# Performance work log

Hardware: AMD Instinct MI355X
Metric: run time of the kernel (lower is better)

Reference implementation:

```python
import jax, jax.numpy as jnp
import numpy as np

D_MODEL = 1024
N_HEADS = 16
D_HEAD = D_MODEL // N_HEADS


def setup_inputs() -> dict:
    key = jax.random.key(0)
    kx, kq, kk, kv = jax.random.split(key, 4)
    B, T = 2, 2048
    X = jax.random.normal(kx, (B, T, D_MODEL), dtype=jnp.float32)
    s = 1.0 / np.sqrt(D_MODEL)
    # torch nn.Linear weight is [out, in]; y = x @ W.T
    Wq = jax.random.uniform(kq, (D_MODEL, D_MODEL), jnp.float32, -s, s)
    Wk = jax.random.uniform(kk, (D_MODEL, D_MODEL), jnp.float32, -s, s)
    Wv = jax.random.uniform(kv, (D_MODEL, D_MODEL), jnp.float32, -s, s)
    return {"X": X, "Wq": Wq, "Wk": Wk, "Wv": Wv}


def reference(X, Wq, Wk, Wv):
    B, T, _ = X.shape
    def heads(W):
        # x @ W.T -> [B,T,D] -> [B,H,T,Dh]
        return (X @ W.T).reshape(B, T, N_HEADS, D_HEAD).transpose(0, 2, 1, 3)
    Q, K, V = heads(Wq), heads(Wk), heads(Wv)
    scores = jnp.einsum('bhqd,bhkd->bhqk', Q, K)
    causal = jnp.tril(jnp.ones((T, T), dtype=bool))
    # original masks with -inf BEFORE scaling; -inf/scale == -inf, so equivalent
    scores = jnp.where(causal, scores, -jnp.inf) / jnp.sqrt(jnp.float32(D_HEAD))
    attn = jax.nn.softmax(scores, axis=-1)
    out = jnp.einsum('bhqk,bhkd->bhqd', attn, V)
    return out.transpose(0, 2, 1, 3).reshape(B, T, N_HEADS * D_HEAD)
```

## Files before the change

### kernel.cpp

```cpp
#include <hip/hip_runtime.h>


using bf16x8   = __attribute__((ext_vector_type(8))) __bf16;
using floatx4  = __attribute__((ext_vector_type(4))) float;
using floatx16 = __attribute__((ext_vector_type(16))) float;
using uintx4   = __attribute__((ext_vector_type(4))) unsigned int;

#define T_SEQ   2048
#define D_MODEL 1024
#define N_HEADS 16
#define D_HEAD  64
#define BATCH   2
#define M_TOT   4096
#define N_TOT   3072
#define PLANE   (T_SEQ * D_HEAD)
#define NX      (M_TOT * D_MODEL)
#define NWSEG   (D_MODEL * D_MODEL)
#define QSCALE  0.18033688f
#define SM_BIAS 24.0f

__device__ __forceinline__ unsigned short f32_to_bf16(float f) {
  unsigned int u = __float_as_uint(f);
  u += 0x7fffu + ((u >> 16) & 1u);
  return (unsigned short)(u >> 16);
}
__device__ __forceinline__ unsigned int pack2_bf16(float a, float b) {
  unsigned int ua = __float_as_uint(a) + 0x8000u;
  unsigned int ub = __float_as_uint(b) + 0x8000u;
  return __builtin_amdgcn_perm(ub, ua, 0x07060302);
}
__device__ __forceinline__ void async_cp16(void* lds, const void* gptr) {
  __builtin_amdgcn_global_load_lds(
      (const __attribute__((address_space(1))) unsigned int*)gptr,
      (__attribute__((address_space(3))) unsigned int*)lds, 16, 0, 0);
}

__global__ __launch_bounds__(256) void cvt_kernel(
    const float* __restrict__ X,  const float* __restrict__ Wq,
    const float* __restrict__ Wk, const float* __restrict__ Wv,
    unsigned short* __restrict__ Xb, unsigned short* __restrict__ Wb)
{
  const size_t i = ((size_t)blockIdx.x * 256 + threadIdx.x) * 8;
  const float* src;
  unsigned short* dst;
  if (i < NX) { src = X + i; dst = Xb + i; }
  else {
    const size_t r = i - NX;
    const int w = (int)(r >> 20);
    const size_t o = r & (NWSEG - 1);
    src = ((w == 0) ? Wq : (w == 1) ? Wk : Wv) + o;
    dst = Wb + r;
  }
  float4 f0 = *(const float4*)src;
  float4 f1 = *(const float4*)(src + 4);
  uint4 out;
  out.x = pack2_bf16(f0.x, f0.y);
  out.y = pack2_bf16(f0.z, f0.w);
  out.z = pack2_bf16(f1.x, f1.y);
  out.w = pack2_bf16(f1.z, f1.w);
  *(uint4*)dst = out;
}

__global__ __launch_bounds__(256) void gemm_qkv(
    const unsigned short* __restrict__ Xb,
    const unsigned short* __restrict__ Wb,
    unsigned short* __restrict__ Qb,
    unsigned short* __restrict__ Kb,
    unsigned short* __restrict__ VTb)
{
  __shared__ unsigned short Als[128 * 64];
  __shared__ unsigned short Bls[128 * 64];

  const int tid  = threadIdx.x;
  const int lane = tid & 63;
  const int wave = tid >> 6;
  const int l15  = lane & 15;
  const int quad = lane >> 4;
  const int wm   = wave >> 1, wn = wave & 1;

  const int n_blk = blockIdx.x * 128;
  const int m_blk = blockIdx.y * 128;

  const int swz = (((tid >> 3) ^ tid) & 7) * 8;
  const unsigned short* Ag = Xb + (size_t)(m_blk + (tid >> 3)) * D_MODEL + swz;
  const unsigned short* Bg = Wb + (size_t)(n_blk + (tid >> 3)) * D_MODEL + swz;
  char* Alds = (char*)Als + wave * 1024;
  char* Blds = (char*)Bls + wave * 1024;

  floatx4 acc[4][4] = {};

  for (int k0 = 0; k0 < D_MODEL; k0 += 64) {
    __syncthreads();
#pragma unroll
    for (int p = 0; p < 4; p++) {
      async_cp16(Alds + p * 4096, Ag + (size_t)p * 32 * D_MODEL + k0);
      async_cp16(Blds + p * 4096, Bg + (size_t)p * 32 * D_MODEL + k0);
    }
    __syncthreads();

#pragma unroll
    for (int ks = 0; ks < 2; ks++) {
      bf16x8 a[4], b[4];
#pragma unroll
      for (int i = 0; i < 4; i++) {
        const int sa = ((ks * 4 + quad) ^ (l15 & 7)) * 16;
        a[i] = *(const bf16x8*)((char*)Als + (wm * 64 + 16 * i + l15) * 128 + sa);
        b[i] = *(const bf16x8*)((char*)Bls + (wn * 64 + 16 * i + l15) * 128 + sa);
      }
#pragma unroll
      for (int mi = 0; mi < 4; mi++)
#pragma unroll
        for (int ni = 0; ni < 4; ni++)
          acc[mi][ni] = __builtin_amdgcn_mfma_f32_16x16x32_bf16(a[mi], b[ni], acc[mi][ni], 0, 0, 0);
    }
  }

  __syncthreads();
  char* ep = (char*)Als + wave * 8192;
  const int w_sel  = n_blk >> 10;
  const int m_base = m_blk + wm * 64;
  const int n_base = n_blk + wn * 64;
  const int h      = (n_base & 1023) >> 6;
  const float csc  = (w_sel == 0) ? QSCALE : 1.0f;

  if (w_sel < 2) {
#pragma unroll
    for (int mi = 0; mi < 4; mi++)
#pragma unroll
      for (int ni = 0; ni < 4; ni++)
#pragma unroll
        for (int r = 0; r < 4; r++) {
          const int row  = 16 * mi + quad * 4 + r;
          const int colb = (16 * ni + l15) * 2;
          const int phys = ((colb >> 4) ^ (row & 7)) * 16;
          *(unsigned short*)(ep + row * 128 + phys + (colb & 15)) =
              f32_to_bf16(acc[mi][ni][r] * csc);
        }
  } else {
#pragma unroll
    for (int mi = 0; mi < 4; mi++)
#pragma unroll
      for (int ni = 0; ni < 4; ni++)
#pragma unroll
        for (int r = 0; r < 4; r++) {
          const int row  = 16 * ni + l15;
          const int colb = (16 * mi + quad * 4 + r) * 2;
          const int phys = ((colb >> 4) ^ (row & 7)) * 16;
          *(unsigned short*)(ep + row * 128 + phys + (colb & 15)) =
              f32_to_bf16(acc[mi][ni][r]);
        }
  }
  asm volatile("s_waitcnt lgkmcnt(0)" ::: "memory");

#pragma unroll
  for (int pass = 0; pass < 8; pass++) {
    const int row  = pass * 8 + (lane >> 3);
    const int phys = ((lane & 7) ^ (row & 7)) * 16;
    uint4 v = *(const uint4*)(ep + row * 128 + phys);
    if (w_sel < 2) {
      const int m  = m_base + row;
      const int bb = m >> 11;
      const int t  = m & (T_SEQ - 1);
      unsigned short* dst = ((w_sel == 0) ? Qb : Kb) +
          ((size_t)(bb * N_HEADS + h) * T_SEQ + t) * D_HEAD + (lane & 7) * 8;
      *(uint4*)dst = v;
    } else {
      const int bb = m_base >> 11;
      unsigned short* dst = VTb +
          ((size_t)(bb * N_HEADS + h) * D_HEAD + row) * T_SEQ + (m_base & (T_SEQ - 1)) + (lane & 7) * 8;
      *(uint4*)dst = v;
    }
  }
}

__global__ __launch_bounds__(256) void attn_kernel(
    const unsigned short* __restrict__ Qb,
    const unsigned short* __restrict__ Kb,
    const unsigned short* __restrict__ VTb,
    float* __restrict__ Out)
{
  __shared__ __align__(16) char smem[65536];

  const int tid  = threadIdx.x;
  const int lane = tid & 63;
  const int wave = tid >> 6;
  const int l31  = lane & 31;
  const int q1   = lane >> 5;
  const int wq   = wave & 1;
  const int wk   = wave >> 1;

  const int bh   = blockIdx.x & 31;
  const int pair = blockIdx.x >> 5;

  const unsigned short* Qp = Qb  + (size_t)bh * PLANE;
  const unsigned short* Kp = Kb  + (size_t)bh * PLANE;
  const unsigned short* Vp = VTb + (size_t)bh * PLANE;
  const int b = bh >> 4, h = bh & 15;

  const int swz = (((tid >> 3) ^ tid) & 7) * 8;
  const unsigned short* Kg = Kp + (size_t)(tid >> 3) * D_HEAD + swz;
  const unsigned short* Vg = Vp + (size_t)(tid >> 3) * T_SEQ + swz;

  float* const LB = (float*)(smem + 33792);

#define STAGE_CHUNK(c)                                                        \
  do {                                                                        \
    char* kd = smem + (((c) >> 1) & 1) * 16384 + ((c) & 1) * 8192;            \
    char* vd = smem + 32768 + (((c) >> 1) & 1) * 16384 + ((c) & 1) * 8192;    \
    _Pragma("unroll")                                                         \
    for (int p = 0; p < 2; p++) {                                             \
      async_cp16(kd + p * 4096 + wave * 1024,                                 \
                 Kg + (size_t)((c) * 64 + p * 32) * D_HEAD);                  \
      async_cp16(vd + p * 4096 + wave * 1024,                                 \
                 Vg + (size_t)(p * 32) * T_SEQ + (c) * 64);                   \
    }                                                                         \
  } while (0)

#pragma unroll 1
  for (int it = 0; it < 2; it++) {
    const int strip = it ? (31 - pair) : pair;
    const int qbase = strip * 64 + wq * 32;
    const int nch   = strip + 1;

    bf16x8 aq[4];
#pragma unroll
    for (int kp = 0; kp < 4; kp++)
      aq[kp] = *(const bf16x8*)(Qp + (size_t)(qbase + l31) * D_HEAD + kp * 16 + q1 * 8);

    floatx16 o0 = {}, o1 = {};
    float l_acc = 0.0f;

    __syncthreads();

    STAGE_CHUNK(0);
    if (nch > 1) STAGE_CHUNK(1);

#pragma unroll 1
    for (int j2 = 0; j2 < nch; j2 += 2) {
      __syncthreads();
      if (j2 + 2 < nch) STAGE_CHUNK(j2 + 2);

#pragma unroll
      for (int u = 0; u < 2; u++) {
        const int jc = j2 + u;
        if (jc >= nch) break;
        if (u == 1 && j2 + 3 < nch) STAGE_CHUNK(j2 + 3);
        const char* Ksb = smem + ((jc >> 1) & 1) * 16384 + (jc & 1) * 8192;
        const char* Vsb = smem + 32768 + ((jc >> 1) & 1) * 16384 + (jc & 1) * 8192;
        const int kbase = jc * 64 + wk * 32;

        if (kbase <= qbase + 31) {
          floatx16 s = {};
          const int krow = wk * 32 + l31;
          __builtin_amdgcn_s_setprio(1);
#pragma unroll
          for (int kp = 0; kp < 4; kp++) {
            const int c = 2 * kp + q1;
            bf16x8 ak = *(const bf16x8*)(Ksb + krow * 128 + ((c ^ (krow & 7)) * 16));
            s = __builtin_amdgcn_mfma_f32_32x32x16_bf16(ak, aq[kp], s, 0, 0, 0);
          }
          __builtin_amdgcn_s_setprio(0);

          if (kbase >= qbase) {
            const int q = qbase + l31;
#pragma unroll
            for (int r = 0; r < 16; r++) {
              const int kk = kbase + (r & 3) + 8 * (r >> 2) + 4 * q1;
              if (kk > q) s[r] = -INFINITY;
            }
          }

          float pv[16];
#pragma unroll
          for (int r = 0; r < 16; r++)
            pv[r] = __builtin_amdgcn_exp2f(s[r] - SM_BIAS);
#pragma unroll
          for (int r = 0; r < 16; r += 4)
            l_acc += (pv[r] + pv[r + 1]) + (pv[r + 2] + pv[r + 3]);

          unsigned int w[8];
#pragma unroll
          for (int m = 0; m < 8; m++)
            asm("v_cvt_pk_bf16_f32 %0, %1, %2" : "=v"(w[m]) : "v"(pv[2 * m]), "v"(pv[2 * m + 1]));

          __builtin_amdgcn_s_setprio(1);
#pragma unroll
          for (int kp = 0; kp < 2; kp++) {
            unsigned int b0 = w[4 * kp],     b2 = w[4 * kp + 2];
            unsigned int b1 = w[4 * kp + 1], b3 = w[4 * kp + 3];
            asm("v_permlane32_swap_b32 %0, %1" : "+v"(b0), "+v"(b2));
            asm("v_permlane32_swap_b32 %0, %1" : "+v"(b1), "+v"(b3));
            uintx4 uu; uu[0] = b0; uu[1] = b1; uu[2] = b2; uu[3] = b3;
            const bf16x8 pf = __builtin_bit_cast(bf16x8, uu);

            const int cv = 4 * wk + 2 * kp + q1;
            bf16x8 av0 = *(const bf16x8*)(Vsb + l31 * 128 + ((cv ^ (l31 & 7)) * 16));
            o0 = __builtin_amdgcn_mfma_f32_32x32x16_bf16(av0, pf, o0, 0, 0, 0);
            const int row1 = 32 + l31;
            bf16x8 av1 = *(const bf16x8*)(Vsb + row1 * 128 + ((cv ^ (row1 & 7)) * 16));
            o1 = __builtin_amdgcn_mfma_f32_32x32x16_bf16(av1, pf, o1, 0, 0, 0);
          }
          __builtin_amdgcn_s_setprio(0);
        }
      }
    }

    float la = l_acc, lb2 = l_acc;
    asm("v_permlane32_swap_b32 %0, %1" : "+v"(la), "+v"(lb2));
    const float lt = la + lb2;

    __syncthreads();

    float* ob = (float*)smem + (wk * 2 + wq) * (64 * 33);
#pragma unroll
    for (int r = 0; r < 16; r++) {
      const int d0 = (r & 3) + 8 * (r >> 2) + 4 * q1;
      ob[d0 * 33 + l31]        = o0[r];
      ob[(32 + d0) * 33 + l31] = o1[r];
    }
    if (lane < 32) LB[wk * 64 + wq * 32 + l31] = lt;
    __syncthreads();

    const int row = tid >> 2;
    const int dg  = tid & 3;
    const int wqr = row >> 5, ql = row & 31;
    const float inv = 1.0f / (LB[row] + LB[64 + row]);
    const float* obA = (const float*)smem + (0 * 2 + wqr) * (64 * 33);
    const float* obB = (const float*)smem + (1 * 2 + wqr) * (64 * 33);

    float vout[16];
#pragma unroll
    for (int i = 0; i < 16; i++) {
      const int d = dg * 16 + i;
      vout[i] = (obA[d * 33 + ql] + obB[d * 33 + ql]) * inv;
    }
    const int t = strip * 64 + row;
    float* dst = Out + (size_t)(b * T_SEQ + t) * D_MODEL + h * D_HEAD + dg * 16;
#pragma unroll
    for (int m = 0; m < 4; m++)
      *(float4*)(dst + 4 * m) = *(const float4*)(vout + 4 * m);
  }
#undef STAGE_CHUNK
}

extern "C" void kernel_launch(void* const* d_in, const int* in_sizes, int n_in,
                              void* d_out, int out_size, void* d_ws, size_t ws_size,
                              hipStream_t stream) {
  const float* X  = (const float*)d_in[0];
  const float* Wq = (const float*)d_in[1];
  const float* Wk = (const float*)d_in[2];
  const float* Wv = (const float*)d_in[3];

  unsigned short* Qb = (unsigned short*)d_ws;
  unsigned short* Kb = Qb + (size_t)BATCH * N_HEADS * T_SEQ * D_HEAD;
  unsigned short* VT = Kb + (size_t)BATCH * N_HEADS * T_SEQ * D_HEAD;

  unsigned short* Xb = (unsigned short*)d_out;
  unsigned short* Wb = Xb + (size_t)NX;

  cvt_kernel<<<3584, 256, 0, stream>>>(X, Wq, Wk, Wv, Xb, Wb);

  dim3 g1(N_TOT / 128, M_TOT / 128);
  gemm_qkv<<<g1, 256, 0, stream>>>(Xb, Wb, Qb, Kb, VT);

  attn_kernel<<<512, 256, 0, stream>>>(Qb, Kb, VT, (float*)d_out);
}
```

Baseline: 151.0 us.

## Use 512-thread blocks in QKV GEMM with 32x64 per-wave tiles

The QKV projection GEMM now runs 8 waves per block instead of 4. Each wave computes a 32x64 sub-tile, which halves the accumulator registers per wave, and the LDS load and epilogue staging are redistributed to match. The goal is more resident waves to hide LDS and global latency. The cost is more fragment loads per MFMA, since each wave reuses B across only two A rows, and a new epilogue swizzle that could be wrong.

```diff
diff --git a/kernel.cpp b/kernel.cpp
--- a/kernel.cpp
+++ b/kernel.cpp
@@ -61,7 +61,7 @@
   *(uint4*)dst = out;
 }
 
-__global__ __launch_bounds__(256) void gemm_qkv(
+__global__ __launch_bounds__(512, 6) void gemm_qkv(
     const unsigned short* __restrict__ Xb,
     const unsigned short* __restrict__ Wb,
     unsigned short* __restrict__ Qb,
@@ -76,7 +76,8 @@
   const int wave = tid >> 6;
   const int l15  = lane & 15;
   const int quad = lane >> 4;
-  const int wm   = wave >> 1, wn = wave & 1;
+  const int wm   = wave & 3;
+  const int wn   = wave >> 2;
 
   const int n_blk = blockIdx.x * 128;
   const int m_blk = blockIdx.y * 128;
@@ -87,28 +88,29 @@
   char* Alds = (char*)Als + wave * 1024;
   char* Blds = (char*)Bls + wave * 1024;
 
-  floatx4 acc[4][4] = {};
+  floatx4 acc[2][4] = {};
 
   for (int k0 = 0; k0 < D_MODEL; k0 += 64) {
     __syncthreads();
 #pragma unroll
-    for (int p = 0; p < 4; p++) {
-      async_cp16(Alds + p * 4096, Ag + (size_t)p * 32 * D_MODEL + k0);
-      async_cp16(Blds + p * 4096, Bg + (size_t)p * 32 * D_MODEL + k0);
+    for (int p = 0; p < 2; p++) {
+      async_cp16(Alds + p * 8192, Ag + (size_t)(p * 64) * D_MODEL + k0);
+      async_cp16(Blds + p * 8192, Bg + (size_t)(p * 64) * D_MODEL + k0);
     }
     __syncthreads();
 
 #pragma unroll
     for (int ks = 0; ks < 2; ks++) {
-      bf16x8 a[4], b[4];
-#pragma unroll
-      for (int i = 0; i < 4; i++) {
-        const int sa = ((ks * 4 + quad) ^ (l15 & 7)) * 16;
-        a[i] = *(const bf16x8*)((char*)Als + (wm * 64 + 16 * i + l15) * 128 + sa);
-        b[i] = *(const bf16x8*)((char*)Bls + (wn * 64 + 16 * i + l15) * 128 + sa);
-      }
-#pragma unroll
-      for (int mi = 0; mi < 4; mi++)
+      bf16x8 a[2], b[4];
+      const int sa = ((ks * 4 + quad) ^ (l15 & 7)) * 16;
+#pragma unroll
+      for (int i = 0; i < 2; i++)
+        a[i] = *(const bf16x8*)((char*)Als + (wm * 32 + 16 * i + l15) * 128 + sa);
+#pragma unroll
+      for (int j = 0; j < 4; j++)
+        b[j] = *(const bf16x8*)((char*)Bls + (wn * 64 + 16 * j + l15) * 128 + sa);
+#pragma unroll
+      for (int mi = 0; mi < 2; mi++)
 #pragma unroll
         for (int ni = 0; ni < 4; ni++)
           acc[mi][ni] = __builtin_amdgcn_mfma_f32_16x16x32_bf16(a[mi], b[ni], acc[mi][ni], 0, 0, 0);
@@ -116,16 +118,17 @@
   }
 
   __syncthreads();
-  char* ep = (char*)Als + wave * 8192;
+  char* ep = (char*)Als + wave * 4096;
   const int w_sel  = n_blk >> 10;
-  const int m_base = m_blk + wm * 64;
+  const int m_base = m_blk + wm * 32;
   const int n_base = n_blk + wn * 64;
   const int h      = (n_base & 1023) >> 6;
   const float csc  = (w_sel == 0) ? QSCALE : 1.0f;
+  const int bb     = m_base >> 11;
 
   if (w_sel < 2) {
 #pragma unroll
-    for (int mi = 0; mi < 4; mi++)
+    for (int mi = 0; mi < 2; mi++)
 #pragma unroll
       for (int ni = 0; ni < 4; ni++)
 #pragma unroll
@@ -138,36 +141,41 @@
         }
   } else {
 #pragma unroll
-    for (int mi = 0; mi < 4; mi++)
+    for (int mi = 0; mi < 2; mi++)
 #pragma unroll
       for (int ni = 0; ni < 4; ni++)
 #pragma unroll
         for (int r = 0; r < 4; r++) {
           const int row  = 16 * ni + l15;
           const int colb = (16 * mi + quad * 4 + r) * 2;
-          const int phys = ((colb >> 4) ^ (row & 7)) * 16;
-          *(unsigned short*)(ep + row * 128 + phys + (colb & 15)) =
+          const int phys = ((colb >> 4) ^ (row & 3)) * 16;
+          *(unsigned short*)(ep + row * 64 + phys + (colb & 15)) =
               f32_to_bf16(acc[mi][ni][r]);
         }
   }
   asm volatile("s_waitcnt lgkmcnt(0)" ::: "memory");
 
-#pragma unroll
-  for (int pass = 0; pass < 8; pass++) {
-    const int row  = pass * 8 + (lane >> 3);
-    const int phys = ((lane & 7) ^ (row & 7)) * 16;
-    uint4 v = *(const uint4*)(ep + row * 128 + phys);
-    if (w_sel < 2) {
-      const int m  = m_base + row;
-      const int bb = m >> 11;
-      const int t  = m & (T_SEQ - 1);
+  if (w_sel < 2) {
+#pragma unroll
+    for (int pass = 0; pass < 4; pass++) {
+      const int row = pass * 8 + (lane >> 3);
+      const int cl  = (lane & 7) ^ (row & 7);
+      uint4 v = *(const uint4*)(ep + row * 128 + (lane & 7) * 16);
+      const int m = m_base + row;
+      const int t = m & (T_SEQ - 1);
       unsigned short* dst = ((w_sel == 0) ? Qb : Kb) +
-          ((size_t)(bb * N_HEADS + h) * T_SEQ + t) * D_HEAD + (lane & 7) * 8;
+          ((size_t)(bb * N_HEADS + h) * T_SEQ + t) * D_HEAD + cl * 8;
       *(uint4*)dst = v;
-    } else {
-      const int bb = m_base >> 11;
+    }
+  } else {
+#pragma unroll
+    for (int pass = 0; pass < 4; pass++) {
+      const int row = pass * 16 + (lane >> 2);
+      const int cl  = (lane & 3) ^ (row & 3);
+      uint4 v = *(const uint4*)(ep + row * 64 + (lane & 3) * 16);
       unsigned short* dst = VTb +
-          ((size_t)(bb * N_HEADS + h) * D_HEAD + row) * T_SEQ + (m_base & (T_SEQ - 1)) + (lane & 7) * 8;
+          ((size_t)(bb * N_HEADS + h) * D_HEAD + row) * T_SEQ +
+          (m_base & (T_SEQ - 1)) + cl * 8;
       *(uint4*)dst = v;
     }
   }
@@ -361,7 +369,7 @@
   cvt_kernel<<<3584, 256, 0, stream>>>(X, Wq, Wk, Wv, Xb, Wb);
 
   dim3 g1(N_TOT / 128, M_TOT / 128);
-  gemm_qkv<<<g1, 256, 0, stream>>>(Xb, Wb, Qb, Kb, VT);
+  gemm_qkv<<<g1, 512, 0, stream>>>(Xb, Wb, Qb, Kb, VT);
 
   attn_kernel<<<512, 256, 0, stream>>>(Qb, Kb, VT, (float*)d_out);
 }
```

After: 139.8 us. -7.4%, faster.
